# Kernel optimization log

Hardware: AMD Instinct MI355X
Metric: run time of the kernel (lower is better)

The kernel has to match this reference:

```python
import jax, jax.numpy as jnp
import numpy as np

N_PARENTS = 8
CHILDREN_PER_PARENT = 7
N_CHILDREN = N_PARENTS * CHILDREN_PER_PARENT  # 56 leaf classes
TOTAL_NODES = N_PARENTS + N_CHILDREN          # 64
BATCH = 262144


def _build_state_space():
    """Faithful port of generate_state_space for levels==2.

    Row 0 is the all-zero root state; then for each parent, one parent-only
    row, followed by one (parent, child) row per child. Shape [65, 64].
    """
    S = np.zeros((TOTAL_NODES + 1, TOTAL_NODES), dtype=np.float32)
    recorded = np.zeros(TOTAL_NODES)
    ii = 1
    for c in range(N_CHILDREN):
        p = N_CHILDREN + c // CHILDREN_PER_PARENT  # parent ids 56..63
        if recorded[p] == 0:
            S[ii, p] = 1.0
            recorded[p] = 1
            ii += 1
        S[ii, p] = 1.0
        S[ii, c] = 1.0
        ii += 1
    assert ii == TOTAL_NODES + 1, 'Invalid State Space'
    return jnp.asarray(S)


def setup_inputs() -> dict:
    key = jax.random.key(0)
    k1, k2 = jax.random.split(key)
    pred_label = jax.random.normal(k1, (BATCH, TOTAL_NODES), dtype=jnp.float32)
    gt_label = jax.random.randint(k2, (BATCH,), 0, N_CHILDREN, dtype=jnp.int32)
    return {
        'pred_label': pred_label,
        'gt_label': gt_label,
        'state_space': _build_state_space(),
    }


def reference(pred_label, gt_label, state_space):
    # index[s, b] = <state_space row s, pred_label[b]>  -> [S+1, B]
    index = state_space @ pred_label.T
    joint = jnp.exp(index)                      # [S+1, B]
    z = jnp.sum(joint, axis=0)                  # [B] partition function
    # Vectorized replacement of the per-sample Python loop:
    # rows of the state space that contain the ground-truth node.
    mask = state_space[:, gt_label] > 0         # [S+1, B]
    marginal = jnp.sum(jnp.where(mask, joint, jnp.zeros((), joint.dtype)), axis=0)  # [B]
    loss = -jnp.log(marginal / z)               # [B]
    return jnp.mean(loss)
```

## Files before the change

kernel.cpp:

```cpp
#include <hip/hip_runtime.h>


#define ROWS_PER_BLOCK 256
#define ROW_PAD 65

__global__ void __launch_bounds__(256) tree_loss_partial(
    const float* __restrict__ pred,
    const int*   __restrict__ gt,
    float*       __restrict__ partial,
    int rows)
{
    __shared__ float lds[ROWS_PER_BLOCK * ROW_PAD];
    __shared__ float wsum[4];

    const int t = threadIdx.x;
    const int rowBase = blockIdx.x * ROWS_PER_BLOCK;

    const float4* p4 = (const float4*)pred + (size_t)rowBase * 16;
    #pragma unroll
    for (int i = 0; i < 16; ++i) {
        int f   = i * 256 + t;
        int row = f >> 4;
        int col = (f & 15) << 2;
        if (rowBase + row < rows) {
            float4 v = p4[f];
            float* dst = &lds[row * ROW_PAD + col];
            dst[0] = __expf(v.x);
            dst[1] = __expf(v.y);
            dst[2] = __expf(v.z);
            dst[3] = __expf(v.w);
        }
    }
    __syncthreads();

    float loss = 0.0f;
    const int rowg = rowBase + t;
    if (rowg < rows) {
        const float* e = &lds[t * ROW_PAD];
        float z = 1.0f;
        #pragma unroll
        for (int p = 0; p < 8; ++p) {
            float s = 1.0f;
            #pragma unroll
            for (int c = 0; c < 7; ++c) s += e[p * 7 + c];
            z += e[56 + p] * s;
        }
        int g = gt[rowg];
        float m = e[g] * e[56 + g / 7];
        loss = __logf(z / m);
    }

    #pragma unroll
    for (int off = 32; off; off >>= 1) loss += __shfl_xor(loss, off);
    const int lane = t & 63, wv = t >> 6;
    if (lane == 0) wsum[wv] = loss;
    __syncthreads();
    if (t == 0) partial[blockIdx.x] = wsum[0] + wsum[1] + wsum[2] + wsum[3];
}

__global__ void __launch_bounds__(256) tree_loss_final(
    const float* __restrict__ partial, int n,
    float* __restrict__ out, float inv)
{
    float s = 0.0f;
    for (int i = threadIdx.x; i < n; i += blockDim.x) s += partial[i];
    #pragma unroll
    for (int off = 32; off; off >>= 1) s += __shfl_xor(s, off);
    __shared__ float w[4];
    const int lane = threadIdx.x & 63;
    const int wv   = threadIdx.x >> 6;
    if (lane == 0) w[wv] = s;
    __syncthreads();
    if (threadIdx.x == 0) out[0] = (w[0] + w[1] + w[2] + w[3]) * inv;
}

extern "C" void kernel_launch(void* const* d_in, const int* in_sizes, int n_in,
                              void* d_out, int out_size, void* d_ws, size_t ws_size,
                              hipStream_t stream) {
    const float* pred = (const float*)d_in[0];
    const int*   gt   = (const int*)d_in[1];
    float* out     = (float*)d_out;
    float* partial = (float*)d_ws;
    const int rows = in_sizes[1];

    int blocks = (rows + ROWS_PER_BLOCK - 1) / ROWS_PER_BLOCK;
    tree_loss_partial<<<blocks, 256, 0, stream>>>(pred, gt, partial, rows);
    tree_loss_final<<<1, 256, 0, stream>>>(partial, blocks, out, 1.0f / (float)rows);
}
```

Before: 22.72 us.

## Fuse final reduction via last-block atomic counter and split row work across 512 threads

Merges the partial and final reduction kernels into one launch: each block publishes its partial sum, increments an atomic counter, and the last block to arrive performs the global reduction. Block size doubles to 512 threads, and each row's partition function is computed as two halves in parallel, combined through shared memory. A hipMemsetAsync is added to reset the counter before each launch. The aim is to remove the second kernel launch and raise per-block parallelism, at the cost of an extra barrier, atomics and a memset operation.

```diff
diff --git a/kernel.cpp b/kernel.cpp
--- a/kernel.cpp
+++ b/kernel.cpp
@@ -1,77 +1,106 @@
 #include <hip/hip_runtime.h>
 
 
-#define ROWS_PER_BLOCK 256
+#define RPB     256
 #define ROW_PAD 65
+#define THREADS 512
 
-__global__ void __launch_bounds__(256) tree_loss_partial(
+__global__ void __launch_bounds__(THREADS) tree_loss_fused(
     const float* __restrict__ pred,
     const int*   __restrict__ gt,
     float*       __restrict__ partial,
-    int rows)
+    int*         __restrict__ counter,
+    float*       __restrict__ out,
+    int rows, float inv)
 {
-    __shared__ float lds[ROWS_PER_BLOCK * ROW_PAD];
-    __shared__ float wsum[4];
+    __shared__ float lds[RPB * ROW_PAD];
+    __shared__ float zhalf[THREADS];
+    __shared__ float wsum[THREADS / 64];
+    __shared__ int   lastFlag;
 
     const int t = threadIdx.x;
-    const int rowBase = blockIdx.x * ROWS_PER_BLOCK;
+    const int rowBase = blockIdx.x * RPB;
+    const bool full = (rowBase + RPB <= rows);
 
     const float4* p4 = (const float4*)pred + (size_t)rowBase * 16;
     #pragma unroll
-    for (int i = 0; i < 16; ++i) {
-        int f   = i * 256 + t;
+    for (int i = 0; i < 8; ++i) {
+        int f   = i * THREADS + t;
         int row = f >> 4;
         int col = (f & 15) << 2;
-        if (rowBase + row < rows) {
+        if (full || rowBase + row < rows) {
             float4 v = p4[f];
             float* dst = &lds[row * ROW_PAD + col];
-            dst[0] = __expf(v.x);
-            dst[1] = __expf(v.y);
-            dst[2] = __expf(v.z);
-            dst[3] = __expf(v.w);
+            dst[0] = __expf(v.x); dst[1] = __expf(v.y);
+            dst[2] = __expf(v.z); dst[3] = __expf(v.w);
         }
     }
     __syncthreads();
 
+    {
+        const int r  = t & (RPB - 1);
+        const int hi = t >> 8;
+        float zh = 0.0f;
+        if (full || rowBase + r < rows) {
+            const float* e  = &lds[r * ROW_PAD];
+            const float* ec = e + hi * 28;
+            const float* ep = e + 56 + hi * 4;
+            #pragma unroll
+            for (int p = 0; p < 4; ++p) {
+                float s = 1.0f;
+                #pragma unroll
+                for (int c = 0; c < 7; ++c) s += ec[p * 7 + c];
+                zh += ep[p] * s;
+            }
+        }
+        zhalf[t] = zh;
+    }
+    __syncthreads();
+
     float loss = 0.0f;
-    const int rowg = rowBase + t;
-    if (rowg < rows) {
-        const float* e = &lds[t * ROW_PAD];
-        float z = 1.0f;
-        #pragma unroll
-        for (int p = 0; p < 8; ++p) {
-            float s = 1.0f;
-            #pragma unroll
-            for (int c = 0; c < 7; ++c) s += e[p * 7 + c];
-            z += e[56 + p] * s;
+    if (t < RPB) {
+        const int rowg = rowBase + t;
+        if (rowg < rows) {
+            float z = 1.0f + zhalf[t] + zhalf[t + RPB];
+            const float* e = &lds[t * ROW_PAD];
+            int g = gt[rowg];
+            float m = e[g] * e[56 + g / 7];
+            loss = __logf(z / m);
         }
-        int g = gt[rowg];
-        float m = e[g] * e[56 + g / 7];
-        loss = __logf(z / m);
     }
-
     #pragma unroll
     for (int off = 32; off; off >>= 1) loss += __shfl_xor(loss, off);
-    const int lane = t & 63, wv = t >> 6;
-    if (lane == 0) wsum[wv] = loss;
+    if ((t & 63) == 0) wsum[t >> 6] = loss;
     __syncthreads();
-    if (t == 0) partial[blockIdx.x] = wsum[0] + wsum[1] + wsum[2] + wsum[3];
-}
 
-__global__ void __launch_bounds__(256) tree_loss_final(
-    const float* __restrict__ partial, int n,
-    float* __restrict__ out, float inv)
-{
-    float s = 0.0f;
-    for (int i = threadIdx.x; i < n; i += blockDim.x) s += partial[i];
-    #pragma unroll
-    for (int off = 32; off; off >>= 1) s += __shfl_xor(s, off);
-    __shared__ float w[4];
-    const int lane = threadIdx.x & 63;
-    const int wv   = threadIdx.x >> 6;
-    if (lane == 0) w[wv] = s;
+    if (t == 0) {
+        float b = 0.0f;
+        #pragma unroll
+        for (int w = 0; w < THREADS / 64; ++w) b += wsum[w];
+        __hip_atomic_store(&partial[blockIdx.x], b,
+                           __ATOMIC_RELEASE, __HIP_MEMORY_SCOPE_AGENT);
+        int old = __hip_atomic_fetch_add(counter, 1,
+                                         __ATOMIC_ACQ_REL, __HIP_MEMORY_SCOPE_AGENT);
+        lastFlag = (old == (int)gridDim.x - 1);
+    }
     __syncthreads();
-    if (threadIdx.x == 0) out[0] = (w[0] + w[1] + w[2] + w[3]) * inv;
+
+    if (lastFlag) {
+        float s = 0.0f;
+        for (int i = t; i < (int)gridDim.x; i += THREADS)
+            s += __hip_atomic_load(&partial[i],
+                                   __ATOMIC_ACQUIRE, __HIP_MEMORY_SCOPE_AGENT);
+        #pragma unroll
+        for (int off = 32; off; off >>= 1) s += __shfl_xor(s, off);
+        if ((t & 63) == 0) wsum[t >> 6] = s;
+        __syncthreads();
+        if (t == 0) {
+            float b = 0.0f;
+            #pragma unroll
+            for (int w = 0; w < THREADS / 64; ++w) b += wsum[w];
+            out[0] = b * inv;
+        }
+    }
 }
 
 extern "C" void kernel_launch(void* const* d_in, const int* in_sizes, int n_in,
@@ -79,11 +108,15 @@
                               hipStream_t stream) {
     const float* pred = (const float*)d_in[0];
     const int*   gt   = (const int*)d_in[1];
-    float* out     = (float*)d_out;
-    float* partial = (float*)d_ws;
+    float* out = (float*)d_out;
     const int rows = in_sizes[1];
 
-    int blocks = (rows + ROWS_PER_BLOCK - 1) / ROWS_PER_BLOCK;
-    tree_loss_partial<<<blocks, 256, 0, stream>>>(pred, gt, partial, rows);
-    tree_loss_final<<<1, 256, 0, stream>>>(partial, blocks, out, 1.0f / (float)rows);
+    const int blocks = (rows + RPB - 1) / RPB;
+    float* partial = (float*)d_ws;
+    int*   counter = (int*)((char*)d_ws + ((size_t)blocks * sizeof(float) + 255 & ~(size_t)255));
+
+    hipMemsetAsync(counter, 0, sizeof(int), stream);
+
+    tree_loss_fused<<<blocks, THREADS, 0, stream>>>(
+        pred, gt, partial, counter, out, rows, 1.0f / (float)rows);
 }
```

Result: slower. 48.16 us (+111.9%).
